# Kernel optimization log

Hardware: AMD Instinct MI355X
Metric: run time of the kernel (lower is better)

## Reference

```python
import jax, jax.numpy as jnp
import numpy as np

NUM_STATION = 20
NUM_HEADS = 8
INPUT_DIM = 128
KEY_DIM = 16          # = val_dim = embed_dim // num_heads
EMBED_DIM = 128
NORM = 1.0 / np.sqrt(KEY_DIM).astype(np.float32)


def setup_inputs() -> dict:
    key = jax.random.key(0)
    ks = jax.random.split(key, 10)
    B, N, D = 32, 1024, INPUT_DIM
    q = jax.random.normal(ks[0], (B, N, D), jnp.float32)
    h = jax.random.normal(ks[1], (B, N, D), jnp.float32)
    stdv_k = 1.0 / np.sqrt(KEY_DIM)      # torch init: uniform(-1/sqrt(last_dim), ...)
    stdv_e = 1.0 / np.sqrt(EMBED_DIM)
    def U(k, shape, s):
        return jax.random.uniform(k, shape, jnp.float32, -s, s)
    pshape = (NUM_HEADS, INPUT_DIM, KEY_DIM)
    return {
        "q": q,
        "h": h,
        "W_query_custom": U(ks[2], pshape, stdv_k),
        "W_query_custom_1": U(ks[3], pshape, stdv_k),
        "W_key_custom": U(ks[4], pshape, stdv_k),
        "W_val_custom": U(ks[5], pshape, stdv_k),
        "W_query_charge_1": U(ks[6], pshape, stdv_k),
        "W_key_charge": U(ks[7], pshape, stdv_k),
        "W_val_charge": U(ks[8], pshape, stdv_k),
        "W_out": U(ks[9], (NUM_HEADS, KEY_DIM, EMBED_DIM), stdv_e),
    }


def reference(q, h, W_query_custom, W_query_custom_1, W_key_custom, W_val_custom,
              W_query_charge_1, W_key_charge, W_val_charge, W_out):
    S = NUM_STATION + 1                      # depot + stations
    h_st, h_tk = h[:, :S], h[:, S:]          # [B,S,D], [B,T,D]
    q_st, q_tk = q[:, :S], q[:, S:]

    proj = lambda x, W: jnp.einsum('bnd,hdk->hbnk', x, W)

    K_c = proj(h_tk, W_key_custom)           # [H,B,T,K]
    V_c = proj(h_tk, W_val_custom)
    K_s = proj(h_st, W_key_charge)           # [H,B,S,K]
    V_s = proj(h_st, W_val_charge)

    # task -> task attention (queries via W_query_custom_1)
    Q_tt = proj(q_tk, W_query_custom_1)
    A_tt = jax.nn.softmax(NORM * jnp.einsum('hbqk,hbtk->hbqt', Q_tt, K_c), axis=-1)
    heads_t = jnp.einsum('hbqt,hbtk->hbqk', A_tt, V_c)

    # task -> station attention (queries via W_query_custom)
    Q_ts = proj(q_tk, W_query_custom)
    A_ts = jax.nn.softmax(NORM * jnp.einsum('hbqk,hbsk->hbqs', Q_ts, K_s), axis=-1)
    heads_t = heads_t + jnp.einsum('hbqs,hbsk->hbqk', A_ts, V_s)

    # station -> task attention (queries via W_query_charge_1)
    Q_st = proj(q_st, W_query_charge_1)
    A_st = jax.nn.softmax(NORM * jnp.einsum('hbqk,hbtk->hbqt', Q_st, K_c), axis=-1)
    heads_s = jnp.einsum('hbqt,hbtk->hbqk', A_st, V_c)

    heads = jnp.concatenate([heads_s, heads_t], axis=2)   # [H,B,N,K]
    out = jnp.einsum('hbnk,hke->bne', heads, W_out)        # [B,N,E]
    return out
```

## Files before the change

### kernel.cpp

```cpp
#include <hip/hip_runtime.h>

typedef __bf16 bf16x8 __attribute__((ext_vector_type(8)));
typedef float f32x4 __attribute__((ext_vector_type(4)));
typedef float f32x16 __attribute__((ext_vector_type(16)));
typedef unsigned int uint32;
typedef unsigned short u16;

#define NST 21
#define TOK 1003
#define SCL 0.3606737602222409f

union U4B { uint4 u; bf16x8 b; };

__device__ __forceinline__ uint32 pkbf(float a, float b) {
  uint32 ua = __float_as_uint(a), ub = __float_as_uint(b);
  ua += 0x7fffu + ((ua >> 16) & 1u);
  ub += 0x7fffu + ((ub >> 16) & 1u);
  return (ua >> 16) | (ub & 0xffff0000u);
}
__device__ __forceinline__ u16 bf1(float a) {
  uint32 u = __float_as_uint(a);
  u += 0x7fffu + ((u >> 16) & 1u);
  return (u16)(u >> 16);
}
__device__ __forceinline__ uint32 pkperm(float lo, float hi) {
  return __builtin_amdgcn_perm(__float_as_uint(hi), __float_as_uint(lo), 0x07060302u);
}

__global__ __launch_bounds__(256) void prep(
    const float* __restrict__ q, const float* __restrict__ hx,
    const float* __restrict__ W0, const float* __restrict__ W1,
    const float* __restrict__ W2, const float* __restrict__ W3,
    const float* __restrict__ W4, const float* __restrict__ Wqst,
    const float* __restrict__ Wks, const float* __restrict__ Wvs,
    u16* __restrict__ qhbf, u16* __restrict__ WtAll, u16* __restrict__ Qm,
    u16* __restrict__ Ks, u16* __restrict__ Vs) {
  int bid = blockIdx.x, tid = threadIdx.x;
  __shared__ float xq2[2][128], xh2[2][128];
  if (bid < 40) {
    int w = bid >> 3, seg = bid & 7;
    const float* W = (w == 0) ? W0 : (w == 1) ? W1 : (w == 2) ? W2
                     : (w == 3) ? W3 : W4;
    u16* dst = WtAll + w * 16384;
#pragma unroll
    for (int it = 0; it < 8; ++it) {
      int i = seg * 2048 + it * 256 + tid;
      int inner = i & 127, outer = i >> 7;
      float v;
      if (w < 4) {
        int h = outer >> 4, k = outer & 15;
        v = W[h * 2048 + inner * 16 + k];
      } else {
        v = W[inner * 128 + outer];
      }
      dst[outer * 128 + inner] = bf1(v);
    }
  } else if (bid < 4136) {
    int i0 = (bid - 40) * 2048 + tid * 8;
    const float* src = (i0 < 4194304) ? (q + i0) : (hx + (i0 - 4194304));
    float4 a = *(const float4*)src;
    float4 b = *(const float4*)(src + 4);
    uint4 o;
    o.x = pkbf(a.x, a.y); o.y = pkbf(a.z, a.w);
    o.z = pkbf(b.x, b.y); o.w = pkbf(b.z, b.w);
    *((uint4*)qhbf + (i0 >> 3)) = o;
  } else {
    int t2 = bid - 4136;
    int sub = tid >> 7, col = tid & 127;
    int hh = col >> 4, k = col & 15;
    int bs2 = t2 * 2 + sub;
    int b2 = bs2 >> 5, s = bs2 & 31;
    if (s < NST) {
      xq2[sub][col] = q[(size_t)(b2 * 1024 + s) * 128 + col];
      xh2[sub][col] = hx[(size_t)(b2 * 1024 + s) * 128 + col];
    }
    __syncthreads();
    if (s < NST) {
      const float* Wq = Wqst + hh * 2048 + k;
      const float* Wk = Wks + hh * 2048 + k;
      const float* Wv = Wvs + hh * 2048 + k;
      float dq = 0.f, dk_ = 0.f, dv = 0.f;
#pragma unroll 8
      for (int d = 0; d < 128; ++d) {
        float xq = xq2[sub][d], xh = xh2[sub][d];
        dq = fmaf(xq, Wq[d * 16], dq);
        dk_ = fmaf(xh, Wk[d * 16], dk_);
        dv = fmaf(xh, Wv[d * 16], dv);
      }
      Qm[(((size_t)hh * 32 + b2) * 1024 + s) * 16 + k] = bf1(dq * SCL);
      Ks[(((size_t)hh * 32 + b2) * 32 + s) * 16 + k] = bf1(dk_);
      Vs[(((size_t)hh * 32 + b2) * 16 + k) * 32 + s] = bf1(dv);
    } else {
      Ks[(((size_t)hh * 32 + b2) * 32 + s) * 16 + k] = 0;
      Vs[(((size_t)hh * 32 + b2) * 16 + k) * 32 + s] = 0;
    }
  }
}

__device__ __forceinline__ void mm_body(const u16* __restrict__ A,
                                        const u16* __restrict__ WtG,
                                        int m0, int mode, void* outp) {
  __shared__ u16 Wl[128 * 136];
  int tid = threadIdx.x;
#pragma unroll
  for (int r = 0; r < 8; ++r) {
    int i = r * 256 + tid;
    int e = i >> 4, j = i & 15;
    *(uint4*)&Wl[e * 136 + j * 8] = *(const uint4*)(WtG + e * 128 + j * 8);
  }
  __syncthreads();
  int wave = tid >> 6, lane = tid & 63;
  int quad = lane >> 4, l15 = lane & 15;
  int mrow = m0 + wave * 16 + l15;

  f32x4 c[8];
#pragma unroll
  for (int nt = 0; nt < 8; ++nt)
#pragma unroll
    for (int r = 0; r < 4; ++r) c[nt][r] = 0.f;

#pragma unroll
  for (int dk = 0; dk < 4; ++dk) {
    U4B af;
    af.u = *(const uint4*)(A + (size_t)mrow * 128 + dk * 32 + quad * 8);
#pragma unroll
    for (int nt = 0; nt < 8; ++nt) {
      U4B bg;
      bg.u = *(const uint4*)&Wl[(nt * 16 + l15) * 136 + dk * 32 + quad * 8];
      c[nt] = __builtin_amdgcn_mfma_f32_16x16x32_bf16(af.b, bg.b, c[nt], 0, 0, 0);
    }
  }
  int gbase = m0 + wave * 16 + quad * 4;
  int bb = gbase >> 10, n0 = gbase & 1023;
  if (mode == 4) {
#pragma unroll
    for (int nt = 0; nt < 8; ++nt)
#pragma unroll
      for (int r = 0; r < 4; ++r)
        ((float*)outp)[(size_t)(gbase + r) * 128 + nt * 16 + l15] = c[nt][r];
  } else if (mode == 3) {
#pragma unroll
    for (int nt = 0; nt < 8; ++nt) {
      uint2 w2 = make_uint2(pkbf(c[nt][0], c[nt][1]), pkbf(c[nt][2], c[nt][3]));
      *(uint2*)((u16*)outp + (((size_t)nt * 32 + bb) * 16 + l15) * 1024 + n0) = w2;
    }
  } else {
    float scale = (mode <= 1) ? SCL : 1.0f;
#pragma unroll
    for (int nt = 0; nt < 8; ++nt)
#pragma unroll
      for (int r = 0; r < 4; ++r) {
        int n = n0 + r;
        if (mode == 0 && n < NST) continue;
        ((u16*)outp)[(((size_t)nt * 32 + bb) * 1024 + n) * 16 + l15] =
            bf1(c[nt][r] * scale);
      }
  }
}

__global__ __launch_bounds__(256) void proj4(
    const u16* __restrict__ qbf, const u16* __restrict__ hbf,
    const u16* __restrict__ WtAll, u16* __restrict__ Qm,
    u16* __restrict__ Qts, u16* __restrict__ Kc, u16* __restrict__ Vc) {
  int mode = blockIdx.x >> 9, mb = blockIdx.x & 511;
  const u16* A = (mode < 2) ? qbf : hbf;
  void* outp = (mode == 0) ? (void*)Qm : (mode == 1) ? (void*)Qts
               : (mode == 2) ? (void*)Kc : (void*)Vc;
  mm_body(A, WtAll + mode * 16384, mb * 64, mode, outp);
}

__global__ __launch_bounds__(256) void outproj(
    const u16* __restrict__ heads, const u16* __restrict__ WtAll,
    float* __restrict__ out) {
  mm_body(heads, WtAll + 4 * 16384, blockIdx.x * 64, 4, out);
}

__global__ __launch_bounds__(256) void attn_main(
    const u16* __restrict__ Qm, const u16* __restrict__ Qts,
    const u16* __restrict__ Kc, const u16* __restrict__ Vc,
    const u16* __restrict__ Ks, const u16* __restrict__ Vs,
    u16* __restrict__ heads) {
  int bx = blockIdx.x;
  int hb = bx & 255, qc = bx >> 8;
  int h = hb >> 5, b = hb & 31;
  int tid = threadIdx.x;
  int wave = tid >> 6, lane = tid & 63;
  int l5 = lane >> 5, l31 = lane & 31;
  int quad = lane >> 4, l15 = lane & 15;

  __shared__ u16 Kl[128 * 26];
  __shared__ u16 Vl[16 * 140];
  __shared__ u16 Pt[4][64 * 36];
  __shared__ u16 KsL[32 * 26];
  __shared__ u16 VsL[16 * 44];

  const u16* Qbase = Qm + ((size_t)(h * 32 + b)) * 16384;
  const u16* QtsB = Qts + ((size_t)(h * 32 + b)) * 16384;
  const u16* Kbase = Kc + ((size_t)(h * 32 + b)) * 16384;
  const u16* Vbase = Vc + ((size_t)(h * 32 + b)) * 16384;
  const u16* KsB = Ks + (size_t)(h * 32 + b) * 512;
  const u16* VsB = Vs + (size_t)(h * 32 + b) * 512;

  if (tid < 64) {
    int key = tid >> 1, half = tid & 1;
    *(uint4*)&KsL[key * 26 + half * 8] = *(const uint4*)(KsB + key * 16 + half * 8);
  } else if (tid < 128) {
    int t = tid - 64;
    int d = t >> 2, kg = t & 3;
    *(uint4*)&VsL[d * 44 + kg * 8] = *(const uint4*)(VsB + d * 32 + kg * 8);
  }

  int qw0 = qc * 256 + wave * 64;
  U4B qf0, qf1;
  qf0.u = *(const uint4*)(Qbase + (size_t)(qw0 + l31) * 16 + l5 * 8);
  qf1.u = *(const uint4*)(Qbase + (size_t)(qw0 + 32 + l31) * 16 + l5 * 8);

  f32x16 zero16;
#pragma unroll
  for (int i = 0; i < 16; ++i) zero16[i] = 0.f;
  U4B ones;
  ones.u = make_uint4(0x3F803F80u, 0x3F803F80u, 0x3F803F80u, 0x3F803F80u);

  f32x4 o[4], la[4];
#pragma unroll
  for (int mt = 0; mt < 4; ++mt)
#pragma unroll
    for (int r = 0; r < 4; ++r) { o[mt][r] = 0.f; la[mt][r] = 0.f; }

#pragma unroll 1
  for (int kb = 0; kb < 8; ++kb) {
    int j0 = kb * 128;
    __syncthreads();
    {
      int key = tid >> 1, half = tid & 1;
      *(uint4*)&Kl[key * 26 + half * 8] =
          *(const uint4*)(Kbase + (size_t)(j0 + key) * 16 + half * 8);
      int d = tid >> 4, kg = tid & 15;
      *(uint4*)&Vl[d * 140 + kg * 8] =
          *(const uint4*)(Vbase + (size_t)d * 1024 + j0 + kg * 8);
    }
    __syncthreads();
#pragma unroll 1
    for (int kt = 0; kt < 4; ++kt) {
      int key0 = kt * 32;
      U4B af;
      af.u = *(const uint4*)&Kl[(key0 + l31) * 26 + l5 * 8];
      f32x16 c0 =
          __builtin_amdgcn_mfma_f32_32x32x16_bf16(af.b, qf0.b, zero16, 0, 0, 0);
      f32x16 c1 =
          __builtin_amdgcn_mfma_f32_32x32x16_bf16(af.b, qf1.b, zero16, 0, 0, 0);
      bool masked = (kb == 0) && (kt == 0);
#pragma unroll
      for (int f = 0; f < 2; ++f) {
        const f32x16& c = f ? c1 : c0;
        int qq = f * 32 + l31;
#pragma unroll
        for (int g = 0; g < 4; ++g) {
          float p0 = __builtin_amdgcn_exp2f(c[4 * g + 0]);
          float p1 = __builtin_amdgcn_exp2f(c[4 * g + 1]);
          float p2 = __builtin_amdgcn_exp2f(c[4 * g + 2]);
          float p3 = __builtin_amdgcn_exp2f(c[4 * g + 3]);
          if (masked) {
            int kb0 = 8 * g + 4 * l5;
            p0 = (kb0 + 0 < NST) ? 0.f : p0;
            p1 = (kb0 + 1 < NST) ? 0.f : p1;
            p2 = (kb0 + 2 < NST) ? 0.f : p2;
            p3 = (kb0 + 3 < NST) ? 0.f : p3;
          }
          uint2 w2 = make_uint2(pkperm(p0, p1), pkperm(p2, p3));
          *(uint2*)&Pt[wave][qq * 36 + 4 * l5 + 8 * g] = w2;
        }
      }
      U4B vf;
      vf.u = *(const uint4*)&Vl[l15 * 140 + key0 + quad * 8];
#pragma unroll
      for (int mt = 0; mt < 4; ++mt) {
        U4B pf;
        pf.u = *(const uint4*)&Pt[wave][(mt * 16 + l15) * 36 + quad * 8];
        o[mt] = __builtin_amdgcn_mfma_f32_16x16x32_bf16(pf.b, vf.b, o[mt], 0, 0, 0);
        la[mt] =
            __builtin_amdgcn_mfma_f32_16x16x32_bf16(pf.b, ones.b, la[mt], 0, 0, 0);
      }
    }
  }

  f32x4 o2[4], la2[4];
#pragma unroll
  for (int mt = 0; mt < 4; ++mt)
#pragma unroll
    for (int r = 0; r < 4; ++r) { o2[mt][r] = 0.f; la2[mt][r] = 0.f; }
  qf0.u = *(const uint4*)(QtsB + (size_t)(qw0 + l31) * 16 + l5 * 8);
  qf1.u = *(const uint4*)(QtsB + (size_t)(qw0 + 32 + l31) * 16 + l5 * 8);
  {
    U4B af;
    af.u = *(const uint4*)&KsL[l31 * 26 + l5 * 8];
    f32x16 c0 =
        __builtin_amdgcn_mfma_f32_32x32x16_bf16(af.b, qf0.b, zero16, 0, 0, 0);
    f32x16 c1 =
        __builtin_amdgcn_mfma_f32_32x32x16_bf16(af.b, qf1.b, zero16, 0, 0, 0);
#pragma unroll
    for (int f = 0; f < 2; ++f) {
      const f32x16& c = f ? c1 : c0;
      int qq = f * 32 + l31;
#pragma unroll
      for (int g = 0; g < 4; ++g) {
        float p0 = __builtin_amdgcn_exp2f(c[4 * g + 0]);
        float p1 = __builtin_amdgcn_exp2f(c[4 * g + 1]);
        float p2 = __builtin_amdgcn_exp2f(c[4 * g + 2]);
        float p3 = __builtin_amdgcn_exp2f(c[4 * g + 3]);
        int kb0 = 8 * g + 4 * l5;
        p0 = (kb0 + 0 >= NST) ? 0.f : p0;
        p1 = (kb0 + 1 >= NST) ? 0.f : p1;
        p2 = (kb0 + 2 >= NST) ? 0.f : p2;
        p3 = (kb0 + 3 >= NST) ? 0.f : p3;
        uint2 w2 = make_uint2(pkperm(p0, p1), pkperm(p2, p3));
        *(uint2*)&Pt[wave][qq * 36 + 4 * l5 + 8 * g] = w2;
      }
    }
    U4B vf;
    vf.u = *(const uint4*)&VsL[l15 * 44 + quad * 8];
#pragma unroll
    for (int mt = 0; mt < 4; ++mt) {
      U4B pf;
      pf.u = *(const uint4*)&Pt[wave][(mt * 16 + l15) * 36 + quad * 8];
      o2[mt] = __builtin_amdgcn_mfma_f32_16x16x32_bf16(pf.b, vf.b, o2[mt], 0, 0, 0);
      la2[mt] =
          __builtin_amdgcn_mfma_f32_16x16x32_bf16(pf.b, ones.b, la2[mt], 0, 0, 0);
    }
  }

#pragma unroll
  for (int mt = 0; mt < 4; ++mt)
#pragma unroll
    for (int r = 0; r < 4; ++r) {
      int n = qw0 + mt * 16 + quad * 4 + r;
      float val = o[mt][r] * __builtin_amdgcn_rcpf(la[mt][r]);
      if (n >= NST) val += o2[mt][r] * __builtin_amdgcn_rcpf(la2[mt][r]);
      heads[((size_t)b * 1024 + n) * 128 + h * 16 + l15] = bf1(val);
    }
}

extern "C" void kernel_launch(void* const* d_in, const int* in_sizes, int n_in,
                              void* d_out, int out_size, void* d_ws,
                              size_t ws_size, hipStream_t stream) {
  (void)in_sizes; (void)n_in; (void)out_size; (void)ws_size;
  const float* q     = (const float*)d_in[0];
  const float* hx    = (const float*)d_in[1];
  const float* W_qts = (const float*)d_in[2];
  const float* W_qtt = (const float*)d_in[3];
  const float* W_kc  = (const float*)d_in[4];
  const float* W_vc  = (const float*)d_in[5];
  const float* W_qst = (const float*)d_in[6];
  const float* W_ks  = (const float*)d_in[7];
  const float* W_vs  = (const float*)d_in[8];
  const float* W_out = (const float*)d_in[9];

  char* ws = (char*)d_ws;
  u16* qhbf  = (u16*)(ws + 0);
  u16* heads = (u16*)(ws + 0);
  u16* hbf   = (u16*)(ws + 8388608);
  u16* Qm    = (u16*)(ws + 16777216);
  u16* Qts   = (u16*)(ws + 25165824);
  u16* Kc    = (u16*)(ws + 33554432);
  u16* Vc    = (u16*)(ws + 41943040);
  u16* Ks    = (u16*)(ws + 50331648);
  u16* Vs    = (u16*)(ws + 50593792);
  u16* WtAll = (u16*)(ws + 50855936);

  hipLaunchKernelGGL(prep, dim3(4648), dim3(256), 0, stream,
                     q, hx, W_qtt, W_qts, W_kc, W_vc, W_out, W_qst, W_ks, W_vs,
                     qhbf, WtAll, Qm, Ks, Vs);
  hipLaunchKernelGGL(proj4, dim3(2048), dim3(256), 0, stream,
                     qhbf, hbf, WtAll, Qm, Qts, Kc, Vc);
  hipLaunchKernelGGL(attn_main, dim3(1024), dim3(256), 0, stream,
                     Qm, Qts, Kc, Vc, Ks, Vs, heads);
  hipLaunchKernelGGL(outproj, dim3(512), dim3(256), 0, stream,
                     heads, WtAll, (float*)d_out);
}
```

Measured before the change: 190.1 us.

## Rewrite attention to register-only 16-query waves reading K/V directly from global

The attention kernel drops its shared-memory staging of K, V and P and the block-wide syncs. Each wave now handles 16 queries with 16x16x32 MFMAs, keeping the probabilities in registers as the B operand of the PV product, and takes row sums with lane shuffles instead of a ones-MFMA. The grid grows fourfold to give more parallelism. The prep kernel's block roles are reordered so the station projection blocks come first, and the weight tile's LDS row padding changes from 136 to 138 to alter bank mapping. The trade-off is more repeated global/L2 traffic for K/V, since each wave reloads them with no reuse across waves.

```diff
diff --git a/kernel.cpp b/kernel.cpp
--- a/kernel.cpp
+++ b/kernel.cpp
@@ -2,12 +2,10 @@
 
 typedef __bf16 bf16x8 __attribute__((ext_vector_type(8)));
 typedef float f32x4 __attribute__((ext_vector_type(4)));
-typedef float f32x16 __attribute__((ext_vector_type(16)));
 typedef unsigned int uint32;
 typedef unsigned short u16;
 
 #define NST 21
-#define TOK 1003
 #define SCL 0.3606737602222409f
 
 union U4B { uint4 u; bf16x8 b; };
@@ -37,35 +35,8 @@
     u16* __restrict__ Ks, u16* __restrict__ Vs) {
   int bid = blockIdx.x, tid = threadIdx.x;
   __shared__ float xq2[2][128], xh2[2][128];
-  if (bid < 40) {
-    int w = bid >> 3, seg = bid & 7;
-    const float* W = (w == 0) ? W0 : (w == 1) ? W1 : (w == 2) ? W2
-                     : (w == 3) ? W3 : W4;
-    u16* dst = WtAll + w * 16384;
-#pragma unroll
-    for (int it = 0; it < 8; ++it) {
-      int i = seg * 2048 + it * 256 + tid;
-      int inner = i & 127, outer = i >> 7;
-      float v;
-      if (w < 4) {
-        int h = outer >> 4, k = outer & 15;
-        v = W[h * 2048 + inner * 16 + k];
-      } else {
-        v = W[inner * 128 + outer];
-      }
-      dst[outer * 128 + inner] = bf1(v);
-    }
-  } else if (bid < 4136) {
-    int i0 = (bid - 40) * 2048 + tid * 8;
-    const float* src = (i0 < 4194304) ? (q + i0) : (hx + (i0 - 4194304));
-    float4 a = *(const float4*)src;
-    float4 b = *(const float4*)(src + 4);
-    uint4 o;
-    o.x = pkbf(a.x, a.y); o.y = pkbf(a.z, a.w);
-    o.z = pkbf(b.x, b.y); o.w = pkbf(b.z, b.w);
-    *((uint4*)qhbf + (i0 >> 3)) = o;
-  } else {
-    int t2 = bid - 4136;
+  if (bid < 512) {
+    int t2 = bid;
     int sub = tid >> 7, col = tid & 127;
     int hh = col >> 4, k = col & 15;
     int bs2 = t2 * 2 + sub;
@@ -94,19 +65,47 @@
       Ks[(((size_t)hh * 32 + b2) * 32 + s) * 16 + k] = 0;
       Vs[(((size_t)hh * 32 + b2) * 16 + k) * 32 + s] = 0;
     }
+  } else if (bid < 552) {
+    int wb = bid - 512;
+    int w = wb >> 3, seg = wb & 7;
+    const float* W = (w == 0) ? W0 : (w == 1) ? W1 : (w == 2) ? W2
+                     : (w == 3) ? W3 : W4;
+    u16* dst = WtAll + w * 16384;
+#pragma unroll
+    for (int it = 0; it < 8; ++it) {
+      int i = seg * 2048 + it * 256 + tid;
+      int inner = i & 127, outer = i >> 7;
+      float v;
+      if (w < 4) {
+        int h = outer >> 4, k = outer & 15;
+        v = W[h * 2048 + inner * 16 + k];
+      } else {
+        v = W[inner * 128 + outer];
+      }
+      dst[outer * 128 + inner] = bf1(v);
+    }
+  } else {
+    int i0 = (bid - 552) * 2048 + tid * 8;
+    const float* src = (i0 < 4194304) ? (q + i0) : (hx + (i0 - 4194304));
+    float4 a = *(const float4*)src;
+    float4 b = *(const float4*)(src + 4);
+    uint4 o;
+    o.x = pkbf(a.x, a.y); o.y = pkbf(a.z, a.w);
+    o.z = pkbf(b.x, b.y); o.w = pkbf(b.z, b.w);
+    *((uint4*)qhbf + (i0 >> 3)) = o;
   }
 }
 
 __device__ __forceinline__ void mm_body(const u16* __restrict__ A,
                                         const u16* __restrict__ WtG,
                                         int m0, int mode, void* outp) {
-  __shared__ u16 Wl[128 * 136];
+  __shared__ u16 Wl[128 * 138];
   int tid = threadIdx.x;
 #pragma unroll
   for (int r = 0; r < 8; ++r) {
     int i = r * 256 + tid;
     int e = i >> 4, j = i & 15;
-    *(uint4*)&Wl[e * 136 + j * 8] = *(const uint4*)(WtG + e * 128 + j * 8);
+    *(uint4*)&Wl[e * 138 + j * 8] = *(const uint4*)(WtG + e * 128 + j * 8);
   }
   __syncthreads();
   int wave = tid >> 6, lane = tid & 63;
@@ -126,7 +125,7 @@
 #pragma unroll
     for (int nt = 0; nt < 8; ++nt) {
       U4B bg;
-      bg.u = *(const uint4*)&Wl[(nt * 16 + l15) * 136 + dk * 32 + quad * 8];
+      bg.u = *(const uint4*)&Wl[(nt * 16 + l15) * 138 + dk * 32 + quad * 8];
       c[nt] = __builtin_amdgcn_mfma_f32_16x16x32_bf16(af.b, bg.b, c[nt], 0, 0, 0);
     }
   }
@@ -185,159 +184,105 @@
   int h = hb >> 5, b = hb & 31;
   int tid = threadIdx.x;
   int wave = tid >> 6, lane = tid & 63;
-  int l5 = lane >> 5, l31 = lane & 31;
   int quad = lane >> 4, l15 = lane & 15;
-
-  __shared__ u16 Kl[128 * 26];
-  __shared__ u16 Vl[16 * 140];
-  __shared__ u16 Pt[4][64 * 36];
-  __shared__ u16 KsL[32 * 26];
-  __shared__ u16 VsL[16 * 44];
-
-  const u16* Qbase = Qm + ((size_t)(h * 32 + b)) * 16384;
-  const u16* QtsB = Qts + ((size_t)(h * 32 + b)) * 16384;
-  const u16* Kbase = Kc + ((size_t)(h * 32 + b)) * 16384;
-  const u16* Vbase = Vc + ((size_t)(h * 32 + b)) * 16384;
-  const u16* KsB = Ks + (size_t)(h * 32 + b) * 512;
-  const u16* VsB = Vs + (size_t)(h * 32 + b) * 512;
-
-  if (tid < 64) {
-    int key = tid >> 1, half = tid & 1;
-    *(uint4*)&KsL[key * 26 + half * 8] = *(const uint4*)(KsB + key * 16 + half * 8);
-  } else if (tid < 128) {
-    int t = tid - 64;
-    int d = t >> 2, kg = t & 3;
-    *(uint4*)&VsL[d * 44 + kg * 8] = *(const uint4*)(VsB + d * 32 + kg * 8);
-  }
-
-  int qw0 = qc * 256 + wave * 64;
-  U4B qf0, qf1;
-  qf0.u = *(const uint4*)(Qbase + (size_t)(qw0 + l31) * 16 + l5 * 8);
-  qf1.u = *(const uint4*)(Qbase + (size_t)(qw0 + 32 + l31) * 16 + l5 * 8);
-
-  f32x16 zero16;
-#pragma unroll
-  for (int i = 0; i < 16; ++i) zero16[i] = 0.f;
-  U4B ones;
-  ones.u = make_uint4(0x3F803F80u, 0x3F803F80u, 0x3F803F80u, 0x3F803F80u);
-
-  f32x4 o[4], la[4];
-#pragma unroll
-  for (int mt = 0; mt < 4; ++mt)
-#pragma unroll
-    for (int r = 0; r < 4; ++r) { o[mt][r] = 0.f; la[mt][r] = 0.f; }
-
-#pragma unroll 1
-  for (int kb = 0; kb < 8; ++kb) {
-    int j0 = kb * 128;
-    __syncthreads();
-    {
-      int key = tid >> 1, half = tid & 1;
-      *(uint4*)&Kl[key * 26 + half * 8] =
-          *(const uint4*)(Kbase + (size_t)(j0 + key) * 16 + half * 8);
-      int d = tid >> 4, kg = tid & 15;
-      *(uint4*)&Vl[d * 140 + kg * 8] =
-          *(const uint4*)(Vbase + (size_t)d * 1024 + j0 + kg * 8);
-    }
-    __syncthreads();
-#pragma unroll 1
-    for (int kt = 0; kt < 4; ++kt) {
-      int key0 = kt * 32;
-      U4B af;
-      af.u = *(const uint4*)&Kl[(key0 + l31) * 26 + l5 * 8];
-      f32x16 c0 =
-          __builtin_amdgcn_mfma_f32_32x32x16_bf16(af.b, qf0.b, zero16, 0, 0, 0);
-      f32x16 c1 =
-          __builtin_amdgcn_mfma_f32_32x32x16_bf16(af.b, qf1.b, zero16, 0, 0, 0);
-      bool masked = (kb == 0) && (kt == 0);
-#pragma unroll
-      for (int f = 0; f < 2; ++f) {
-        const f32x16& c = f ? c1 : c0;
-        int qq = f * 32 + l31;
-#pragma unroll
-        for (int g = 0; g < 4; ++g) {
-          float p0 = __builtin_amdgcn_exp2f(c[4 * g + 0]);
-          float p1 = __builtin_amdgcn_exp2f(c[4 * g + 1]);
-          float p2 = __builtin_amdgcn_exp2f(c[4 * g + 2]);
-          float p3 = __builtin_amdgcn_exp2f(c[4 * g + 3]);
-          if (masked) {
-            int kb0 = 8 * g + 4 * l5;
-            p0 = (kb0 + 0 < NST) ? 0.f : p0;
-            p1 = (kb0 + 1 < NST) ? 0.f : p1;
-            p2 = (kb0 + 2 < NST) ? 0.f : p2;
-            p3 = (kb0 + 3 < NST) ? 0.f : p3;
-          }
-          uint2 w2 = make_uint2(pkperm(p0, p1), pkperm(p2, p3));
-          *(uint2*)&Pt[wave][qq * 36 + 4 * l5 + 8 * g] = w2;
-        }
-      }
-      U4B vf;
-      vf.u = *(const uint4*)&Vl[l15 * 140 + key0 + quad * 8];
-#pragma unroll
-      for (int mt = 0; mt < 4; ++mt) {
-        U4B pf;
-        pf.u = *(const uint4*)&Pt[wave][(mt * 16 + l15) * 36 + quad * 8];
-        o[mt] = __builtin_amdgcn_mfma_f32_16x16x32_bf16(pf.b, vf.b, o[mt], 0, 0, 0);
-        la[mt] =
-            __builtin_amdgcn_mfma_f32_16x16x32_bf16(pf.b, ones.b, la[mt], 0, 0, 0);
-      }
-    }
-  }
-
-  f32x4 o2[4], la2[4];
-#pragma unroll
-  for (int mt = 0; mt < 4; ++mt)
-#pragma unroll
-    for (int r = 0; r < 4; ++r) { o2[mt][r] = 0.f; la2[mt][r] = 0.f; }
-  qf0.u = *(const uint4*)(QtsB + (size_t)(qw0 + l31) * 16 + l5 * 8);
-  qf1.u = *(const uint4*)(QtsB + (size_t)(qw0 + 32 + l31) * 16 + l5 * 8);
+  int q8 = (quad & 1) * 8;
+  int xq = quad * 4;
+
+  const u16* Qbase = Qm + (size_t)hb * 16384;
+  const u16* Kbase = Kc + (size_t)hb * 16384;
+  const u16* Vbase = Vc + (size_t)hb * 16384;
+  const u16* QtsB = Qts + (size_t)hb * 16384;
+  const u16* KsB = Ks + (size_t)hb * 512;
+  const u16* VsB = Vs + (size_t)hb * 512;
+
+  int qw0 = qc * 64 + wave * 16;
+
+  U4B qf;
+  qf.u = make_uint4(0u, 0u, 0u, 0u);
+  if (lane < 32) qf.u = *(const uint4*)(Qbase + (size_t)(qw0 + l15) * 16 + q8);
+
+  f32x4 zero4 = {0.f, 0.f, 0.f, 0.f};
+  f32x4 o = zero4, o2 = zero4;
+  float lsum = 0.f, ls2 = 0.f;
+
   {
-    U4B af;
-    af.u = *(const uint4*)&KsL[l31 * 26 + l5 * 8];
-    f32x16 c0 =
-        __builtin_amdgcn_mfma_f32_32x32x16_bf16(af.b, qf0.b, zero16, 0, 0, 0);
-    f32x16 c1 =
-        __builtin_amdgcn_mfma_f32_32x32x16_bf16(af.b, qf1.b, zero16, 0, 0, 0);
-#pragma unroll
-    for (int f = 0; f < 2; ++f) {
-      const f32x16& c = f ? c1 : c0;
-      int qq = f * 32 + l31;
-#pragma unroll
-      for (int g = 0; g < 4; ++g) {
-        float p0 = __builtin_amdgcn_exp2f(c[4 * g + 0]);
-        float p1 = __builtin_amdgcn_exp2f(c[4 * g + 1]);
-        float p2 = __builtin_amdgcn_exp2f(c[4 * g + 2]);
-        float p3 = __builtin_amdgcn_exp2f(c[4 * g + 3]);
-        int kb0 = 8 * g + 4 * l5;
-        p0 = (kb0 + 0 >= NST) ? 0.f : p0;
-        p1 = (kb0 + 1 >= NST) ? 0.f : p1;
-        p2 = (kb0 + 2 >= NST) ? 0.f : p2;
-        p3 = (kb0 + 3 >= NST) ? 0.f : p3;
-        uint2 w2 = make_uint2(pkperm(p0, p1), pkperm(p2, p3));
-        *(uint2*)&Pt[wave][qq * 36 + 4 * l5 + 8 * g] = w2;
-      }
-    }
-    U4B vf;
-    vf.u = *(const uint4*)&VsL[l15 * 44 + quad * 8];
-#pragma unroll
-    for (int mt = 0; mt < 4; ++mt) {
-      U4B pf;
-      pf.u = *(const uint4*)&Pt[wave][(mt * 16 + l15) * 36 + quad * 8];
-      o2[mt] = __builtin_amdgcn_mfma_f32_16x16x32_bf16(pf.b, vf.b, o2[mt], 0, 0, 0);
-      la2[mt] =
-          __builtin_amdgcn_mfma_f32_16x16x32_bf16(pf.b, ones.b, la2[mt], 0, 0, 0);
-    }
-  }
-
-#pragma unroll
-  for (int mt = 0; mt < 4; ++mt)
+    U4B ae, ao, av;
+    ae.u = *(const uint4*)(Kbase + (size_t)(2 * l15) * 16 + q8);
+    ao.u = *(const uint4*)(Kbase + (size_t)(2 * l15 + 1) * 16 + q8);
+    av.u = *(const uint4*)(Vbase + (size_t)l15 * 1024 + quad * 8);
+    f32x4 ce = __builtin_amdgcn_mfma_f32_16x16x32_bf16(ae.b, qf.b, zero4, 0, 0, 0);
+    f32x4 co = __builtin_amdgcn_mfma_f32_16x16x32_bf16(ao.b, qf.b, zero4, 0, 0, 0);
+    float pe[4], po[4];
 #pragma unroll
     for (int r = 0; r < 4; ++r) {
-      int n = qw0 + mt * 16 + quad * 4 + r;
-      float val = o[mt][r] * __builtin_amdgcn_rcpf(la[mt][r]);
-      if (n >= NST) val += o2[mt][r] * __builtin_amdgcn_rcpf(la2[mt][r]);
-      heads[((size_t)b * 1024 + n) * 128 + h * 16 + l15] = bf1(val);
-    }
+      pe[r] = (xq + r <= 10) ? 0.f : __builtin_amdgcn_exp2f(ce[r]);
+      po[r] = (xq + r <= 9) ? 0.f : __builtin_amdgcn_exp2f(co[r]);
+    }
+    lsum += ((pe[0] + po[0]) + (pe[1] + po[1])) + ((pe[2] + po[2]) + (pe[3] + po[3]));
+    U4B pk;
+    pk.u.x = pkperm(pe[0], po[0]); pk.u.y = pkperm(pe[1], po[1]);
+    pk.u.z = pkperm(pe[2], po[2]); pk.u.w = pkperm(pe[3], po[3]);
+    o = __builtin_amdgcn_mfma_f32_16x16x32_bf16(av.b, pk.b, o, 0, 0, 0);
+  }
+#pragma unroll 2
+  for (int s = 1; s < 32; ++s) {
+    int j0 = s * 32;
+    U4B ae, ao, av;
+    ae.u = *(const uint4*)(Kbase + (size_t)(j0 + 2 * l15) * 16 + q8);
+    ao.u = *(const uint4*)(Kbase + (size_t)(j0 + 2 * l15 + 1) * 16 + q8);
+    av.u = *(const uint4*)(Vbase + (size_t)l15 * 1024 + j0 + quad * 8);
+    f32x4 ce = __builtin_amdgcn_mfma_f32_16x16x32_bf16(ae.b, qf.b, zero4, 0, 0, 0);
+    f32x4 co = __builtin_amdgcn_mfma_f32_16x16x32_bf16(ao.b, qf.b, zero4, 0, 0, 0);
+    float pe[4], po[4];
+#pragma unroll
+    for (int r = 0; r < 4; ++r) {
+      pe[r] = __builtin_amdgcn_exp2f(ce[r]);
+      po[r] = __builtin_amdgcn_exp2f(co[r]);
+    }
+    lsum += ((pe[0] + po[0]) + (pe[1] + po[1])) + ((pe[2] + po[2]) + (pe[3] + po[3]));
+    U4B pk;
+    pk.u.x = pkperm(pe[0], po[0]); pk.u.y = pkperm(pe[1], po[1]);
+    pk.u.z = pkperm(pe[2], po[2]); pk.u.w = pkperm(pe[3], po[3]);
+    o = __builtin_amdgcn_mfma_f32_16x16x32_bf16(av.b, pk.b, o, 0, 0, 0);
+  }
+
+  {
+    U4B q2;
+    q2.u = make_uint4(0u, 0u, 0u, 0u);
+    if (lane < 32) q2.u = *(const uint4*)(QtsB + (size_t)(qw0 + l15) * 16 + q8);
+    U4B ae, ao, av;
+    ae.u = *(const uint4*)(KsB + (2 * l15) * 16 + q8);
+    ao.u = *(const uint4*)(KsB + (2 * l15 + 1) * 16 + q8);
+    av.u = *(const uint4*)(VsB + l15 * 32 + quad * 8);
+    f32x4 ce = __builtin_amdgcn_mfma_f32_16x16x32_bf16(ae.b, q2.b, zero4, 0, 0, 0);
+    f32x4 co = __builtin_amdgcn_mfma_f32_16x16x32_bf16(ao.b, q2.b, zero4, 0, 0, 0);
+    float pe[4], po[4];
+#pragma unroll
+    for (int r = 0; r < 4; ++r) {
+      pe[r] = (xq + r >= 11) ? 0.f : __builtin_amdgcn_exp2f(ce[r]);
+      po[r] = (xq + r >= 10) ? 0.f : __builtin_amdgcn_exp2f(co[r]);
+    }
+    ls2 += ((pe[0] + po[0]) + (pe[1] + po[1])) + ((pe[2] + po[2]) + (pe[3] + po[3]));
+    U4B pk;
+    pk.u.x = pkperm(pe[0], po[0]); pk.u.y = pkperm(pe[1], po[1]);
+    pk.u.z = pkperm(pe[2], po[2]); pk.u.w = pkperm(pe[3], po[3]);
+    o2 = __builtin_amdgcn_mfma_f32_16x16x32_bf16(av.b, pk.b, o2, 0, 0, 0);
+  }
+
+  lsum += __shfl_xor(lsum, 16, 64);
+  lsum += __shfl_xor(lsum, 32, 64);
+  ls2 += __shfl_xor(ls2, 16, 64);
+  ls2 += __shfl_xor(ls2, 32, 64);
+  int n = qw0 + l15;
+  float inv1 = __builtin_amdgcn_rcpf(lsum);
+  float inv2 = __builtin_amdgcn_rcpf(ls2);
+  float v0 = o[0] * inv1, v1 = o[1] * inv1, v2 = o[2] * inv1, v3 = o[3] * inv1;
+  if (n >= NST) {
+    v0 += o2[0] * inv2; v1 += o2[1] * inv2;
+    v2 += o2[2] * inv2; v3 += o2[3] * inv2;
+  }
+  uint2 w2 = make_uint2(pkbf(v0, v1), pkbf(v2, v3));
+  *(uint2*)(heads + ((size_t)b * 1024 + n) * 128 + h * 16 + quad * 4) = w2;
 }
 
 extern "C" void kernel_launch(void* const* d_in, const int* in_sizes, int n_in,
@@ -372,7 +317,7 @@
                      qhbf, WtAll, Qm, Ks, Vs);
   hipLaunchKernelGGL(proj4, dim3(2048), dim3(256), 0, stream,
                      qhbf, hbf, WtAll, Qm, Qts, Kc, Vc);
-  hipLaunchKernelGGL(attn_main, dim3(1024), dim3(256), 0, stream,
+  hipLaunchKernelGGL(attn_main, dim3(4096), dim3(256), 0, stream,
                      Qm, Qts, Kc, Vc, Ks, Vs, heads);
   hipLaunchKernelGGL(outproj, dim3(512), dim3(256), 0, stream,
                      heads, WtAll, (float*)d_out);
```

Result: slower. 281.4 us (+48.0%).
